# Kernel optimization log

Measured on AMD Instinct MI355X. Metric: run time of the kernel, lower is better.

## Reference

```python
import jax, jax.numpy as jnp
import numpy as np

B, S, D, H = 4, 2048, 1024, 16
DK = D // H

def setup_inputs() -> dict:
    key = jax.random.key(0)
    ks = jax.random.split(key, 5)
    x = jax.random.normal(ks[0], (B, S, D), dtype=jnp.float32)
    scale = 1.0 / np.sqrt(D)
    Wq = jax.random.normal(ks[1], (D, D), dtype=jnp.float32) * scale
    Wk = jax.random.normal(ks[2], (D, D), dtype=jnp.float32) * scale
    Wv = jax.random.normal(ks[3], (D, D), dtype=jnp.float32) * scale
    Wo = jax.random.normal(ks[4], (D, D), dtype=jnp.float32) * scale
    return {"x": x, "Wq": Wq, "Wk": Wk, "Wv": Wv, "Wo": Wo}

def reference(x, Wq, Wk, Wv, Wo):
    # F.linear: y = x @ W.T  (weights stored torch-style [out, in])
    q = jnp.einsum('bsd,ed->bse', x, Wq).reshape(B, S, H, DK).transpose(0, 2, 1, 3)
    k = jnp.einsum('bsd,ed->bse', x, Wk).reshape(B, S, H, DK).transpose(0, 2, 1, 3)
    v = jnp.einsum('bsd,ed->bse', x, Wv).reshape(B, S, H, DK).transpose(0, 2, 1, 3)
    scores = jnp.einsum('bhqd,bhkd->bhqk', q, k) / jnp.sqrt(jnp.float32(DK))
    attn = jax.nn.softmax(scores, axis=-1)  # dropout p=0.0 -> identity
    out = jnp.einsum('bhqk,bhkd->bhqd', attn, v)
    out = out.transpose(0, 2, 1, 3).reshape(B, S, D)
    return jnp.einsum('bsd,ed->bse', out, Wo)
```

## Files before the change

### kernel.cpp

```cpp
#include <hip/hip_runtime.h>
#include <hip/hip_bf16.h>

#define B_ 4
#define S_ 2048
#define D_ 1024
#define H_ 16
#define DK_ 64

typedef __attribute__((ext_vector_type(8))) short short8;
typedef __attribute__((ext_vector_type(4))) float floatx4;
typedef __attribute__((ext_vector_type(16))) float floatx16;
typedef __attribute__((ext_vector_type(4))) unsigned int uint4v;

#define QSCL 0.1803368801111204f

static __device__ __forceinline__ unsigned short f2bf(float f) {
    unsigned int u = __float_as_uint(f);
    u += 0x7fffu + ((u >> 16) & 1u);
    return (unsigned short)(u >> 16);
}

static __device__ __forceinline__ unsigned int pack2bf_perm(float a, float b) {
    unsigned int u0 = __float_as_uint(a) + 0x8000u;
    unsigned int u1 = __float_as_uint(b) + 0x8000u;
    return __builtin_amdgcn_perm(u1, u0, 0x07060302u);
}

static __device__ __forceinline__ unsigned int pack2bf(float a, float b) {
    return (unsigned int)f2bf(a) | ((unsigned int)f2bf(b) << 16);
}

#define PLSWAP(a, b) asm volatile("v_permlane32_swap_b32 %0, %1" : "+v"(a), "+v"(b))

struct CastAll {
    const float* x;
    const float* w[4];
    unsigned short* xd;
    unsigned short* wd[4];
};

__global__ void cast_all_kernel(CastAll a) {
    int i = blockIdx.x * blockDim.x + threadIdx.x;
    const float* s;
    unsigned short* d;
    int j;
    if (i < 2097152) {
        s = a.x; d = a.xd; j = i;
    } else {
        int k = i - 2097152;
        int w = k >> 18;
        j = k & 262143;
        s = a.w[w]; d = a.wd[w];
    }
    float4 v = ((const float4*)s)[j];
    ushort4 o;
    o.x = f2bf(v.x); o.y = f2bf(v.y); o.z = f2bf(v.z); o.w = f2bf(v.w);
    ((ushort4*)d)[j] = o;
}

template <typename OutT, bool VT2>
__global__ __launch_bounds__(256) void gemm_bt(
    const unsigned short* __restrict__ A,
    const unsigned short* __restrict__ W0,
    const unsigned short* __restrict__ W1,
    const unsigned short* __restrict__ W2,
    OutT* __restrict__ C0, OutT* __restrict__ C1, OutT* __restrict__ C2,
    int M, int N, int K)
{
    __shared__ __align__(16) unsigned short At[128 * 64];
    __shared__ __align__(16) unsigned short Bt[128 * 64];

    const unsigned short* W = (blockIdx.z == 0) ? W0 : ((blockIdx.z == 1) ? W1 : W2);
    OutT* C = (blockIdx.z == 0) ? C0 : ((blockIdx.z == 1) ? C1 : C2);

    const int n0 = blockIdx.x * 128;
    const int m0 = blockIdx.y * 128;
    const int wv = threadIdx.x >> 6;
    const int ln = threadIdx.x & 63;
    const int l31 = ln & 31;
    const int half = ln >> 5;
    const int wm = (wv >> 1) * 64;
    const int wn = (wv & 1) * 64;

    floatx16 acc[2][2];
#pragma unroll
    for (int mt = 0; mt < 2; mt++)
#pragma unroll
        for (int nt = 0; nt < 2; nt++)
#pragma unroll
            for (int e = 0; e < 16; e++) acc[mt][nt][e] = 0.f;

    const int lr = ln >> 3;
    const int lc = (((ln & 7) ^ lr) * 8);
    const int sw = (l31 & 7);

    for (int k0 = 0; k0 < K; k0 += 64) {
        __syncthreads();
#pragma unroll
        for (int c = 0; c < 4; c++) {
            int rowA = wv * 32 + c * 8;
            const unsigned short* gA = A + (size_t)(m0 + rowA + lr) * K + k0 + lc;
            __builtin_amdgcn_global_load_lds(
                (const __attribute__((address_space(1))) void*)gA,
                (__attribute__((address_space(3))) void*)&At[rowA * 64], 16, 0, 0);
            const unsigned short* gB = W + (size_t)(n0 + rowA + lr) * K + k0 + lc;
            __builtin_amdgcn_global_load_lds(
                (const __attribute__((address_space(1))) void*)gB,
                (__attribute__((address_space(3))) void*)&Bt[rowA * 64], 16, 0, 0);
        }
        __syncthreads();

#pragma unroll
        for (int ks = 0; ks < 4; ks++) {
            const int slot = ((ks * 2 + half) ^ sw) * 8;
            short8 af[2], bf[2];
#pragma unroll
            for (int mt = 0; mt < 2; mt++)
                af[mt] = *(const short8*)&At[(wm + mt * 32 + l31) * 64 + slot];
#pragma unroll
            for (int nt = 0; nt < 2; nt++)
                bf[nt] = *(const short8*)&Bt[(wn + nt * 32 + l31) * 64 + slot];
#pragma unroll
            for (int mt = 0; mt < 2; mt++)
#pragma unroll
                for (int nt = 0; nt < 2; nt++)
                    acc[mt][nt] = __builtin_amdgcn_mfma_f32_32x32x16_bf16(af[mt], bf[nt], acc[mt][nt], 0, 0, 0);
        }
    }

    const float esc = (VT2 && blockIdx.z == 0) ? QSCL : 1.0f;

    if constexpr (VT2) {
        if (blockIdx.z == 2) {
            unsigned short* Vt = (unsigned short*)C;
#pragma unroll
            for (int mt = 0; mt < 2; mt++)
#pragma unroll
                for (int nt = 0; nt < 2; nt++)
#pragma unroll
                    for (int rg = 0; rg < 4; rg++) {
                        int col = n0 + wn + nt * 32 + l31;
                        int row0 = m0 + wm + mt * 32 + 4 * half + 8 * rg;
                        int bb = row0 >> 11, ss = row0 & 2047;
                        size_t addr = ((size_t)(bb * 1024 + col)) * 2048 + ss;
                        uint2 pk;
                        pk.x = pack2bf(acc[mt][nt][4 * rg + 0], acc[mt][nt][4 * rg + 1]);
                        pk.y = pack2bf(acc[mt][nt][4 * rg + 2], acc[mt][nt][4 * rg + 3]);
                        *(uint2*)(Vt + addr) = pk;
                    }
            return;
        }
    }

#pragma unroll
    for (int mt = 0; mt < 2; mt++)
#pragma unroll
        for (int nt = 0; nt < 2; nt++)
#pragma unroll
            for (int rg = 0; rg < 4; rg++)
#pragma unroll
                for (int r = 0; r < 4; r++) {
                    int row = m0 + wm + mt * 32 + 4 * half + 8 * rg + r;
                    int col = n0 + wn + nt * 32 + l31;
                    float v = acc[mt][nt][4 * rg + r] * esc;
                    if constexpr (sizeof(OutT) == 2)
                        C[(size_t)row * N + col] = (OutT)f2bf(v);
                    else
                        C[(size_t)row * N + col] = v;
                }
}

__global__ __launch_bounds__(256, 2) void flash_attn(
    const unsigned short* __restrict__ Q,
    const unsigned short* __restrict__ K,
    const unsigned short* __restrict__ Vt,
    unsigned short* __restrict__ O)
{
    __shared__ __align__(16) unsigned short Kt[64 * 72];
    __shared__ __align__(16) unsigned short VT[64 * 72];

    const int qt = blockIdx.x;
    const int h = blockIdx.y;
    const int b = blockIdx.z;
    const int tid = threadIdx.x;
    const int wv = tid >> 6;
    const int ln = tid & 63;
    const int l31 = ln & 31;
    const int half = ln >> 5;

    const size_t base = ((size_t)b * S_) * D_ + (size_t)h * DK_;
    const size_t vtbase = ((size_t)(b * 1024 + h * 64)) * (size_t)S_;

    const int qrow0 = qt * 256 + wv * 64 + l31;
    short8 qf[2][4];
#pragma unroll
    for (int qh = 0; qh < 2; qh++) {
        const unsigned short* qp = Q + base + (size_t)(qrow0 + qh * 32) * D_ + half * 8;
#pragma unroll
        for (int ks = 0; ks < 4; ks++) qf[qh][ks] = *(const short8*)(qp + ks * 16);
    }

    floatx16 Oacc[2][2];
#pragma unroll
    for (int qh = 0; qh < 2; qh++)
#pragma unroll
        for (int mt = 0; mt < 2; mt++)
#pragma unroll
            for (int e = 0; e < 16; e++) Oacc[qh][mt][e] = 0.f;
    float l_i[2] = {0.f, 0.f};

    const int srow = tid >> 3;
    const int scol = (tid & 7) * 8;
    const unsigned short* kp0 = K + base + (size_t)srow * D_ + scol;
    const unsigned short* kp1 = kp0 + (size_t)32 * D_;
    const unsigned short* vp0 = Vt + vtbase + (size_t)srow * S_ + scol;
    const unsigned short* vp1 = vp0 + (size_t)32 * S_;

    for (int kt = 0; kt < S_ / 64; kt++) {
        __syncthreads();
        *(short8*)&Kt[srow * 72 + scol] = *(const short8*)kp0;
        *(short8*)&Kt[(srow + 32) * 72 + scol] = *(const short8*)kp1;
        *(short8*)&VT[srow * 72 + scol] = *(const short8*)vp0;
        *(short8*)&VT[(srow + 32) * 72 + scol] = *(const short8*)vp1;
        kp0 += (size_t)64 * D_; kp1 += (size_t)64 * D_;
        vp0 += 64; vp1 += 64;
        __syncthreads();

        uint2 run[2][2][4];

#pragma unroll
        for (int mt = 0; mt < 2; mt++) {
            floatx16 sac[2];
#pragma unroll
            for (int qh = 0; qh < 2; qh++)
#pragma unroll
                for (int e = 0; e < 16; e++) sac[qh][e] = 0.f;
#pragma unroll
            for (int ks = 0; ks < 4; ks++) {
                short8 kf = *(const short8*)&Kt[(mt * 32 + l31) * 72 + ks * 16 + half * 8];
                sac[0] = __builtin_amdgcn_mfma_f32_32x32x16_bf16(kf, qf[0][ks], sac[0], 0, 0, 0);
                sac[1] = __builtin_amdgcn_mfma_f32_32x32x16_bf16(kf, qf[1][ks], sac[1], 0, 0, 0);
            }
#pragma unroll
            for (int qh = 0; qh < 2; qh++)
#pragma unroll
                for (int g = 0; g < 4; g++) {
                    float p0 = __builtin_amdgcn_exp2f(sac[qh][4 * g + 0]);
                    float p1 = __builtin_amdgcn_exp2f(sac[qh][4 * g + 1]);
                    float p2 = __builtin_amdgcn_exp2f(sac[qh][4 * g + 2]);
                    float p3 = __builtin_amdgcn_exp2f(sac[qh][4 * g + 3]);
                    l_i[qh] += (p0 + p1) + (p2 + p3);
                    run[qh][mt][g].x = pack2bf_perm(p0, p1);
                    run[qh][mt][g].y = pack2bf_perm(p2, p3);
                }
        }

#pragma unroll
        for (int qh = 0; qh < 2; qh++)
#pragma unroll
            for (int mt = 0; mt < 2; mt++)
#pragma unroll
                for (int t = 0; t < 2; t++) {
                    PLSWAP(run[qh][mt][2 * t].x, run[qh][mt][2 * t + 1].x);
                    PLSWAP(run[qh][mt][2 * t].y, run[qh][mt][2 * t + 1].y);
                }

#pragma unroll
        for (int mt2 = 0; mt2 < 2; mt2++)
#pragma unroll
            for (int t = 0; t < 2; t++) {
                int ks = mt2 * 2 + t;
                short8 pf[2];
#pragma unroll
                for (int qh = 0; qh < 2; qh++) {
                    uint4v u = {run[qh][mt2][2 * t].x, run[qh][mt2][2 * t].y,
                                run[qh][mt2][2 * t + 1].x, run[qh][mt2][2 * t + 1].y};
                    pf[qh] = __builtin_bit_cast(short8, u);
                }
#pragma unroll
                for (int mt = 0; mt < 2; mt++) {
                    short8 vf = *(const short8*)&VT[(mt * 32 + l31) * 72 + ks * 16 + half * 8];
                    Oacc[0][mt] = __builtin_amdgcn_mfma_f32_32x32x16_bf16(vf, pf[0], Oacc[0][mt], 0, 0, 0);
                    Oacc[1][mt] = __builtin_amdgcn_mfma_f32_32x32x16_bf16(vf, pf[1], Oacc[1][mt], 0, 0, 0);
                }
            }
    }

#pragma unroll
    for (int qh = 0; qh < 2; qh++) {
        float ls = l_i[qh] + __shfl_xor(l_i[qh], 32);
        float inv = 1.0f / ls;
        const size_t orow = base + (size_t)(qrow0 + qh * 32) * D_;
#pragma unroll
        for (int mt = 0; mt < 2; mt++)
#pragma unroll
            for (int g = 0; g < 4; g++) {
                uint2 pk;
                pk.x = pack2bf(Oacc[qh][mt][4 * g + 0] * inv, Oacc[qh][mt][4 * g + 1] * inv);
                pk.y = pack2bf(Oacc[qh][mt][4 * g + 2] * inv, Oacc[qh][mt][4 * g + 3] * inv);
                *(uint2*)(O + orow + mt * 32 + 8 * g + 4 * half) = pk;
            }
    }
}

extern "C" void kernel_launch(void* const* d_in, const int* in_sizes, int n_in,
                              void* d_out, int out_size, void* d_ws, size_t ws_size,
                              hipStream_t stream) {
    const float* x  = (const float*)d_in[0];
    const float* Wq = (const float*)d_in[1];
    const float* Wk = (const float*)d_in[2];
    const float* Wv = (const float*)d_in[3];
    const float* Wo = (const float*)d_in[4];
    float* out = (float*)d_out;

    char* ws = (char*)d_ws;
    const size_t MB = 1024 * 1024;
    unsigned short* xb  = (unsigned short*)(ws);
    unsigned short* wqb = (unsigned short*)(ws + 16 * MB);
    unsigned short* wkb = (unsigned short*)(ws + 18 * MB);
    unsigned short* wvb = (unsigned short*)(ws + 20 * MB);
    unsigned short* wob = (unsigned short*)(ws + 22 * MB);
    unsigned short* Qb  = (unsigned short*)(ws + 24 * MB);
    unsigned short* Kb  = (unsigned short*)(ws + 40 * MB);
    unsigned short* Vtb = (unsigned short*)(ws + 56 * MB);
    unsigned short* Ob  = (unsigned short*)(ws);

    CastAll ca;
    ca.x = x; ca.xd = xb;
    ca.w[0] = Wq; ca.w[1] = Wk; ca.w[2] = Wv; ca.w[3] = Wo;
    ca.wd[0] = wqb; ca.wd[1] = wkb; ca.wd[2] = wvb; ca.wd[3] = wob;
    cast_all_kernel<<<12288, 256, 0, stream>>>(ca);

    dim3 gq(D_ / 128, (B_ * S_) / 128, 3);
    gemm_bt<unsigned short, true><<<gq, 256, 0, stream>>>(
        xb, wqb, wkb, wvb, Qb, Kb, Vtb, B_ * S_, D_, D_);

    dim3 gf(S_ / 256, H_, B_);
    flash_attn<<<gf, 256, 0, stream>>>(Qb, Kb, Vtb, Ob);

    dim3 go(D_ / 128, (B_ * S_) / 128, 1);
    gemm_bt<float, false><<<go, 256, 0, stream>>>(
        Ob, wob, wob, wob, out, out, out, B_ * S_, D_, D_);
}
```

Before: 280.1 us.

## Double-buffer K/V tiles with register prefetch and raise MFMA wave priority

The K and V shared-memory tiles are double-buffered, and the next tile is loaded from global memory into registers while the current tile is being computed. This removes one barrier per iteration and hides global load latency behind the MFMA work. The MFMA sections are also wrapped in s_setprio so waves issuing matrix ops get scheduling priority. The cost is twice the LDS per block and extra registers for the prefetched values, which could reduce occupancy at 2 blocks per CU.

```diff
diff --git a/kernel.cpp b/kernel.cpp
--- a/kernel.cpp
+++ b/kernel.cpp
@@ -176,8 +176,8 @@
     const unsigned short* __restrict__ Vt,
     unsigned short* __restrict__ O)
 {
-    __shared__ __align__(16) unsigned short Kt[64 * 72];
-    __shared__ __align__(16) unsigned short VT[64 * 72];
+    __shared__ __align__(16) unsigned short Kt[2][64 * 72];
+    __shared__ __align__(16) unsigned short VT[2][64 * 72];
 
     const int qt = blockIdx.x;
     const int h = blockIdx.y;
@@ -215,16 +215,33 @@
     const unsigned short* kp1 = kp0 + (size_t)32 * D_;
     const unsigned short* vp0 = Vt + vtbase + (size_t)srow * S_ + scol;
     const unsigned short* vp1 = vp0 + (size_t)32 * S_;
+    const int swo = srow * 72 + scol;
+
+    short8 kr0 = *(const short8*)kp0;
+    short8 kr1 = *(const short8*)kp1;
+    short8 vr0 = *(const short8*)vp0;
+    short8 vr1 = *(const short8*)vp1;
+    kp0 += (size_t)64 * D_; kp1 += (size_t)64 * D_;
+    vp0 += 64; vp1 += 64;
 
     for (int kt = 0; kt < S_ / 64; kt++) {
+        const int cb = kt & 1;
+        unsigned short* Kc = &Kt[cb][0];
+        unsigned short* Vc = &VT[cb][0];
+        *(short8*)&Kc[swo] = kr0;
+        *(short8*)&Kc[swo + 32 * 72] = kr1;
+        *(short8*)&Vc[swo] = vr0;
+        *(short8*)&Vc[swo + 32 * 72] = vr1;
         __syncthreads();
-        *(short8*)&Kt[srow * 72 + scol] = *(const short8*)kp0;
-        *(short8*)&Kt[(srow + 32) * 72 + scol] = *(const short8*)kp1;
-        *(short8*)&VT[srow * 72 + scol] = *(const short8*)vp0;
-        *(short8*)&VT[(srow + 32) * 72 + scol] = *(const short8*)vp1;
-        kp0 += (size_t)64 * D_; kp1 += (size_t)64 * D_;
-        vp0 += 64; vp1 += 64;
-        __syncthreads();
+
+        if (kt < S_ / 64 - 1) {
+            kr0 = *(const short8*)kp0;
+            kr1 = *(const short8*)kp1;
+            vr0 = *(const short8*)vp0;
+            vr1 = *(const short8*)vp1;
+            kp0 += (size_t)64 * D_; kp1 += (size_t)64 * D_;
+            vp0 += 64; vp1 += 64;
+        }
 
         uint2 run[2][2][4];
 
@@ -235,12 +252,14 @@
             for (int qh = 0; qh < 2; qh++)
 #pragma unroll
                 for (int e = 0; e < 16; e++) sac[qh][e] = 0.f;
+            __builtin_amdgcn_s_setprio(1);
 #pragma unroll
             for (int ks = 0; ks < 4; ks++) {
-                short8 kf = *(const short8*)&Kt[(mt * 32 + l31) * 72 + ks * 16 + half * 8];
+                short8 kf = *(const short8*)&Kc[(mt * 32 + l31) * 72 + ks * 16 + half * 8];
                 sac[0] = __builtin_amdgcn_mfma_f32_32x32x16_bf16(kf, qf[0][ks], sac[0], 0, 0, 0);
                 sac[1] = __builtin_amdgcn_mfma_f32_32x32x16_bf16(kf, qf[1][ks], sac[1], 0, 0, 0);
             }
+            __builtin_amdgcn_s_setprio(0);
 #pragma unroll
             for (int qh = 0; qh < 2; qh++)
 #pragma unroll
@@ -277,12 +296,14 @@
                                 run[qh][mt2][2 * t + 1].x, run[qh][mt2][2 * t + 1].y};
                     pf[qh] = __builtin_bit_cast(short8, u);
                 }
+                __builtin_amdgcn_s_setprio(1);
 #pragma unroll
                 for (int mt = 0; mt < 2; mt++) {
-                    short8 vf = *(const short8*)&VT[(mt * 32 + l31) * 72 + ks * 16 + half * 8];
+                    short8 vf = *(const short8*)&Vc[(mt * 32 + l31) * 72 + ks * 16 + half * 8];
                     Oacc[0][mt] = __builtin_amdgcn_mfma_f32_32x32x16_bf16(vf, pf[0], Oacc[0][mt], 0, 0, 0);
                     Oacc[1][mt] = __builtin_amdgcn_mfma_f32_32x32x16_bf16(vf, pf[1], Oacc[1][mt], 0, 0, 0);
                 }
+                __builtin_amdgcn_s_setprio(0);
             }
     }
 
```

Result: no change. 283.8 us (+1.3%).
